# Optimization experiments

Hardware: AMD Instinct MI355X
Metric: run time of the kernel (lower is better)

The kernel has to match this reference:

```python
import jax, jax.numpy as jnp
import numpy as np

NUM_LEVELS = 16
FEATS_PER_LEVEL = 2
LOG2_HASHMAP = 19
TABLE_SIZE = 1 << LOG2_HASHMAP
BASE_RES = 16
DESIRED_RES = 4096
PER_LEVEL_SCALE = float(np.exp(np.log(DESIRED_RES / BASE_RES) / (NUM_LEVELS - 1)))
PRIMES = (np.uint32(1), np.uint32(2654435761), np.uint32(805459861))
N_POINTS = 2_000_000


def _level_features(x, table, level):
    # x: [N,3] in [0,1]; table: [TABLE_SIZE, F]
    scale = BASE_RES * (PER_LEVEL_SCALE ** level) - 1.0
    res = int(np.ceil(scale)) + 1
    dense = (res ** 3) <= TABLE_SIZE  # tcnn uses dense indexing when grid fits
    pos = x * scale + 0.5
    pos0 = jnp.floor(pos)
    w = pos - pos0                     # trilinear weights, [N,3]
    base = pos0.astype(jnp.uint32)
    out = jnp.zeros((x.shape[0], table.shape[1]), dtype=table.dtype)
    for c in range(8):                 # 8 corners of the voxel
        offs = [(c >> d) & 1 for d in range(3)]
        pc = [jnp.minimum(base[:, d] + np.uint32(offs[d]), np.uint32(res - 1)) for d in range(3)]
        if dense:
            idx = pc[0] + pc[1] * np.uint32(res) + pc[2] * np.uint32(res * res)
        else:
            idx = (pc[0] * PRIMES[0]) ^ (pc[1] * PRIMES[1]) ^ (pc[2] * PRIMES[2])
            idx = idx & np.uint32(TABLE_SIZE - 1)
        wt = jnp.ones(x.shape[0], dtype=x.dtype)
        for d in range(3):
            wt = wt * (w[:, d] if offs[d] else (1.0 - w[:, d]))
        out = out + wt[:, None] * table[idx.astype(jnp.int32)]
    return out


def hashgrid_encode(x, tables):
    # x: [N,3] in [0,1]; tables: [L, TABLE_SIZE, F] -> [N, L*F]
    return jnp.concatenate(
        [_level_features(x, tables[l], l) for l in range(NUM_LEVELS)], axis=-1)


def setup_inputs() -> dict:
    key = jax.random.key(0)
    k1, k2, k3, k4, k5 = jax.random.split(key, 5)
    points = jax.random.uniform(k1, (N_POINTS, 3), dtype=jnp.float32)
    # tcnn hashgrid init: uniform(-1e-4, 1e-4)
    tables = jax.random.uniform(k2, (NUM_LEVELS, TABLE_SIZE, FEATS_PER_LEVEL),
                                minval=-1e-4, maxval=1e-4, dtype=jnp.float32)
    def kaiming(k, fan_out, fan_in):
        bound = np.sqrt(2.0) * np.sqrt(3.0 / fan_in)
        return jax.random.uniform(k, (fan_out, fan_in), minval=-bound, maxval=bound,
                                  dtype=jnp.float32)
    W1 = kaiming(k3, 32, 32)
    W2 = kaiming(k4, 32, 32)
    W3 = kaiming(k5, 4, 32)
    aabb = jnp.stack([jnp.zeros(3, jnp.float32), jnp.ones(3, jnp.float32)])
    return {"points": points, "tables": tables, "W1": W1, "W2": W2, "W3": W3,
            "aabb": aabb}


def reference(points, tables, W1, W2, W3, aabb):
    texc = jnp.clip((points - aabb[0][None, :]) / (aabb[1] - aabb[0])[None, :], 0.0, 1.0)
    enc = hashgrid_encode(texc, tables)            # [N, 32]
    h = jax.nn.relu(enc @ W1.T)
    h = jax.nn.relu(h @ W2.T)
    out = h @ W3.T                                 # [N, 4]
    mn = jnp.array([0.0, 0.0, 0.0, 0.01], dtype=out.dtype)
    mx = jnp.array([1.0, 1.0, 1.0, 1.0], dtype=out.dtype)
    return jax.nn.sigmoid(out) * (mx - mn) + mn
```

## Files before the change

kernel.cpp:

```cpp
#include <hip/hip_runtime.h>
#include <cmath>


namespace {
constexpr int kLevels = 16;
constexpr unsigned kTableSize = 1u << 19;
constexpr unsigned kMask = kTableSize - 1u;
constexpr int kNumCells = 1 << 18;
constexpr int kScanBlocks = kNumCells / 256;

typedef _Float16 half2_t __attribute__((ext_vector_type(2)));
typedef unsigned int u32;

struct LevelParams {
  float scale[kLevels];
  unsigned res[kLevels];
  int dense[kLevels];
};
}

__device__ __forceinline__ u32 part1by2(u32 x) {
  x &= 0x3FFu;
  x = (x | (x << 16)) & 0x030000FFu;
  x = (x | (x << 8))  & 0x0300F00Fu;
  x = (x | (x << 4))  & 0x030C30C3u;
  x = (x | (x << 2))  & 0x09249249u;
  return x;
}

__device__ __forceinline__ u32 cell_of(float x, float y, float z) {
  u32 cx = min((u32)(x * 64.f), 63u);
  u32 cy = min((u32)(y * 64.f), 63u);
  u32 cz = min((u32)(z * 64.f), 63u);
  return part1by2(cx) | (part1by2(cy) << 1) | (part1by2(cz) << 2);
}

__global__ __launch_bounds__(256)
void conv_tables_kernel(const float2* __restrict__ src, half2_t* __restrict__ dst,
                        int n_entries,
                        const float* __restrict__ W1, const float* __restrict__ W2,
                        const float* __restrict__ W3, half2_t* __restrict__ Wh)
{
  int i = blockIdx.x * blockDim.x + threadIdx.x;
  if (i < 512) {
    Wh[i] = half2_t{(_Float16)W1[2 * i], (_Float16)W1[2 * i + 1]};
  } else if (i < 1024) {
    int t = i - 512;
    Wh[512 + t] = half2_t{(_Float16)W2[2 * t], (_Float16)W2[2 * t + 1]};
  } else if (i < 1088) {
    int t = i - 1024;
    Wh[1024 + t] = half2_t{(_Float16)W3[2 * t], (_Float16)W3[2 * t + 1]};
  }
  int stride = gridDim.x * blockDim.x;
  for (; i < n_entries; i += stride) {
    float2 v = src[i];
    dst[i] = half2_t{(_Float16)v.x, (_Float16)v.y};
  }
}

__global__ __launch_bounds__(256)
void hist_kernel(const float* __restrict__ points, const float* __restrict__ aabb,
                 u32* __restrict__ hist, int n)
{
  int i = blockIdx.x * blockDim.x + threadIdx.x;
  if (i >= n) return;
  float a0x = aabb[0], a0y = aabb[1], a0z = aabb[2];
  float a1x = aabb[3], a1y = aabb[4], a1z = aabb[5];
  float x = fminf(fmaxf((points[3 * i + 0] - a0x) / (a1x - a0x), 0.f), 1.f);
  float y = fminf(fmaxf((points[3 * i + 1] - a0y) / (a1y - a0y), 0.f), 1.f);
  float z = fminf(fmaxf((points[3 * i + 2] - a0z) / (a1z - a0z), 0.f), 1.f);
  atomicAdd(&hist[cell_of(x, y, z)], 1u);
}

__global__ __launch_bounds__(256)
void scan1_kernel(u32* __restrict__ hist, u32* __restrict__ totals)
{
  __shared__ u32 s[256];
  int t = threadIdx.x;
  int base = blockIdx.x * 256;
  u32 v = hist[base + t];
  s[t] = v;
  __syncthreads();
  #pragma unroll
  for (int off = 1; off < 256; off <<= 1) {
    u32 a = (t >= off) ? s[t - off] : 0u;
    __syncthreads();
    s[t] += a;
    __syncthreads();
  }
  if (t == 255) totals[blockIdx.x] = s[255];
  hist[base + t] = s[t] - v;
}

__global__ __launch_bounds__(1024)
void scan2_kernel(u32* __restrict__ totals)
{
  __shared__ u32 s[kScanBlocks];
  int t = threadIdx.x;
  u32 v = totals[t];
  s[t] = v;
  __syncthreads();
  #pragma unroll
  for (int off = 1; off < kScanBlocks; off <<= 1) {
    u32 a = (t >= off) ? s[t - off] : 0u;
    __syncthreads();
    s[t] += a;
    __syncthreads();
  }
  totals[t] = s[t] - v;
}

__global__ __launch_bounds__(256)
void scan3_kernel(u32* __restrict__ hist, const u32* __restrict__ totals)
{
  int t = threadIdx.x;
  int base = blockIdx.x * 256;
  hist[base + t] += totals[blockIdx.x];
}

__global__ __launch_bounds__(256)
void scatter_kernel(const float* __restrict__ points, const float* __restrict__ aabb,
                    u32* __restrict__ offs,
                    float* __restrict__ sx, float* __restrict__ sy,
                    float* __restrict__ sz, u32* __restrict__ perm, int n)
{
  int i = blockIdx.x * blockDim.x + threadIdx.x;
  if (i >= n) return;
  float a0x = aabb[0], a0y = aabb[1], a0z = aabb[2];
  float a1x = aabb[3], a1y = aabb[4], a1z = aabb[5];
  float x = fminf(fmaxf((points[3 * i + 0] - a0x) / (a1x - a0x), 0.f), 1.f);
  float y = fminf(fmaxf((points[3 * i + 1] - a0y) / (a1y - a0y), 0.f), 1.f);
  float z = fminf(fmaxf((points[3 * i + 2] - a0z) / (a1z - a0z), 0.f), 1.f);
  u32 pos = atomicAdd(&offs[cell_of(x, y, z)], 1u);
  sx[pos] = x; sy[pos] = y; sz[pos] = z;
  perm[pos] = (u32)i;
}

__device__ __forceinline__ u32 sel4(uint4 v, u32 j) {
  u32 lo = (j & 1u) ? v.y : v.x;
  u32 hi = (j & 1u) ? v.w : v.z;
  return (j & 2u) ? hi : lo;
}

__global__ __launch_bounds__(256)
void encode_sorted_kernel(const float* __restrict__ sx, const float* __restrict__ sy,
                          const float* __restrict__ sz,
                          const u32* __restrict__ tables,
                          half2_t* __restrict__ enc,
                          LevelParams lp, int n, int bpl)
{
  int l = blockIdx.x / bpl;
  int i = (blockIdx.x - l * bpl) * blockDim.x + threadIdx.x;
  if (i >= n) return;

  float x = sx[i], y = sy[i], z = sz[i];

  float s = lp.scale[l];
  unsigned res = lp.res[l];
  bool dense = (lp.dense[l] != 0);
  unsigned rm1 = res - 1u;
  unsigned res2 = res * res;
  const u32* tab = tables + (size_t)l * kTableSize;

  float fx = x * s + 0.5f, fy = y * s + 0.5f, fz = z * s + 0.5f;
  float fx0 = floorf(fx), fy0 = floorf(fy), fz0 = floorf(fz);
  float wx = fx - fx0, wy = fy - fy0, wz = fz - fz0;
  unsigned bx = (unsigned)fx0, by = (unsigned)fy0, bz = (unsigned)fz0;

  unsigned pcx0 = min(bx, rm1), pcx1 = min(bx + 1u, rm1);

  u32 idx0[4], idx1[4];
  #pragma unroll
  for (int p = 0; p < 4; ++p) {
    unsigned oy = (unsigned)(p & 1);
    unsigned oz = (unsigned)(p >> 1);
    unsigned pcy = min(by + oy, rm1);
    unsigned pcz = min(bz + oz, rm1);
    if (dense) {
      u32 b = pcy * res + pcz * res2;
      idx0[p] = pcx0 + b;
      idx1[p] = pcx1 + b;
    } else {
      u32 h = (pcy * 2654435761u) ^ (pcz * 805459861u);
      idx0[p] = (pcx0 ^ h) & kMask;
      idx1[p] = (pcx1 ^ h) & kMask;
    }
  }

  uint4 v[4];
  #pragma unroll
  for (int p = 0; p < 4; ++p)
    v[p] = *reinterpret_cast<const uint4*>(tab + (idx0[p] & ~3u));

  u32 e1x[4] = {0u, 0u, 0u, 0u};
  #pragma unroll
  for (int p = 0; p < 4; ++p) {
    if ((idx0[p] ^ idx1[p]) >= 4u) e1x[p] = tab[idx1[p]];
  }

  float wx1 = wx, wx0 = 1.f - wx;
  float acc0 = 0.f, acc1 = 0.f;
  #pragma unroll
  for (int p = 0; p < 4; ++p) {
    unsigned oy = (unsigned)(p & 1);
    unsigned oz = (unsigned)(p >> 1);
    float wyz = (oy ? wy : 1.f - wy) * (oz ? wz : 1.f - wz);
    u32 e0 = sel4(v[p], idx0[p] & 3u);
    u32 e1g = sel4(v[p], idx1[p] & 3u);
    u32 e1 = ((idx0[p] ^ idx1[p]) < 4u) ? e1g : e1x[p];
    half2_t f0 = __builtin_bit_cast(half2_t, e0);
    half2_t f1 = __builtin_bit_cast(half2_t, e1);
    float w0 = wyz * wx0, w1 = wyz * wx1;
    acc0 += w0 * (float)f0.x + w1 * (float)f1.x;
    acc1 += w0 * (float)f0.y + w1 * (float)f1.y;
  }
  enc[(size_t)l * n + i] = half2_t{(_Float16)acc0, (_Float16)acc1};
}

__device__ __forceinline__ float dot2_acc(half2_t a, half2_t b, float c) {
#if __has_builtin(__builtin_amdgcn_fdot2)
  return __builtin_amdgcn_fdot2(a, b, c, false);
#else
  return c + (float)a.x * (float)b.x + (float)a.y * (float)b.y;
#endif
}

__global__ __launch_bounds__(256)
void mlp_kernel(const half2_t* __restrict__ enc,
                const half2_t* __restrict__ Wh,
                const u32* __restrict__ perm,
                float* __restrict__ out, int n)
{
  int i = blockIdx.x * blockDim.x + threadIdx.x;
  if (i >= n) return;

  half2_t e[16];
  #pragma unroll
  for (int l = 0; l < kLevels; ++l) e[l] = enc[(size_t)l * n + i];

  const half2_t* W1h = Wh;
  const half2_t* W2h = Wh + 512;
  const half2_t* W3h = Wh + 1024;

  float h1f[32];
  #pragma unroll
  for (int j = 0; j < 32; ++j) {
    float acc = 0.f;
    #pragma unroll
    for (int k = 0; k < 16; ++k) acc = dot2_acc(e[k], W1h[16 * j + k], acc);
    h1f[j] = fmaxf(acc, 0.f);
  }
  half2_t h1[16];
  #pragma unroll
  for (int k = 0; k < 16; ++k)
    h1[k] = half2_t{(_Float16)h1f[2 * k], (_Float16)h1f[2 * k + 1]};

  float h2f[32];
  #pragma unroll
  for (int j = 0; j < 32; ++j) {
    float acc = 0.f;
    #pragma unroll
    for (int k = 0; k < 16; ++k) acc = dot2_acc(h1[k], W2h[16 * j + k], acc);
    h2f[j] = fmaxf(acc, 0.f);
  }
  half2_t h2[16];
  #pragma unroll
  for (int k = 0; k < 16; ++k)
    h2[k] = half2_t{(_Float16)h2f[2 * k], (_Float16)h2f[2 * k + 1]};

  float o[4];
  #pragma unroll
  for (int j = 0; j < 4; ++j) {
    float acc = 0.f;
    #pragma unroll
    for (int k = 0; k < 16; ++k) acc = dot2_acc(h2[k], W3h[16 * j + k], acc);
    o[j] = acc;
  }

  float4 r;
  r.x = 1.f / (1.f + __expf(-o[0]));
  r.y = 1.f / (1.f + __expf(-o[1]));
  r.z = 1.f / (1.f + __expf(-o[2]));
  r.w = 0.99f / (1.f + __expf(-o[3])) + 0.01f;
  int oi = perm ? (int)perm[i] : i;
  reinterpret_cast<float4*>(out)[oi] = r;
}

__global__ __launch_bounds__(256)
void encode_raw_kernel(const float* __restrict__ points,
                       const u32* __restrict__ tables,
                       const float* __restrict__ aabb,
                       half2_t* __restrict__ enc,
                       LevelParams lp, int n, int bpl)
{
  int l = blockIdx.x / bpl;
  int i = (blockIdx.x - l * bpl) * blockDim.x + threadIdx.x;
  if (i >= n) return;

  float a0x = aabb[0], a0y = aabb[1], a0z = aabb[2];
  float a1x = aabb[3], a1y = aabb[4], a1z = aabb[5];
  float x = fminf(fmaxf((points[3 * i + 0] - a0x) / (a1x - a0x), 0.f), 1.f);
  float y = fminf(fmaxf((points[3 * i + 1] - a0y) / (a1y - a0y), 0.f), 1.f);
  float z = fminf(fmaxf((points[3 * i + 2] - a0z) / (a1z - a0z), 0.f), 1.f);

  float s = lp.scale[l];
  unsigned res = lp.res[l];
  bool dense = (lp.dense[l] != 0);
  unsigned rm1 = res - 1u;
  unsigned res2 = res * res;
  const u32* tab = tables + (size_t)l * kTableSize;

  float fx = x * s + 0.5f, fy = y * s + 0.5f, fz = z * s + 0.5f;
  float fx0 = floorf(fx), fy0 = floorf(fy), fz0 = floorf(fz);
  float wx = fx - fx0, wy = fy - fy0, wz = fz - fz0;
  unsigned bx = (unsigned)fx0, by = (unsigned)fy0, bz = (unsigned)fz0;
  unsigned pcx0 = min(bx, rm1), pcx1 = min(bx + 1u, rm1);

  u32 idx0[4], idx1[4];
  #pragma unroll
  for (int p = 0; p < 4; ++p) {
    unsigned oy = (unsigned)(p & 1);
    unsigned oz = (unsigned)(p >> 1);
    unsigned pcy = min(by + oy, rm1);
    unsigned pcz = min(bz + oz, rm1);
    if (dense) {
      u32 b = pcy * res + pcz * res2;
      idx0[p] = pcx0 + b;
      idx1[p] = pcx1 + b;
    } else {
      u32 h = (pcy * 2654435761u) ^ (pcz * 805459861u);
      idx0[p] = (pcx0 ^ h) & kMask;
      idx1[p] = (pcx1 ^ h) & kMask;
    }
  }
  uint4 v[4];
  #pragma unroll
  for (int p = 0; p < 4; ++p)
    v[p] = *reinterpret_cast<const uint4*>(tab + (idx0[p] & ~3u));
  u32 e1x[4] = {0u, 0u, 0u, 0u};
  #pragma unroll
  for (int p = 0; p < 4; ++p) {
    if ((idx0[p] ^ idx1[p]) >= 4u) e1x[p] = tab[idx1[p]];
  }
  float wx1 = wx, wx0 = 1.f - wx;
  float acc0 = 0.f, acc1 = 0.f;
  #pragma unroll
  for (int p = 0; p < 4; ++p) {
    unsigned oy = (unsigned)(p & 1);
    unsigned oz = (unsigned)(p >> 1);
    float wyz = (oy ? wy : 1.f - wy) * (oz ? wz : 1.f - wz);
    u32 e0 = sel4(v[p], idx0[p] & 3u);
    u32 e1g = sel4(v[p], idx1[p] & 3u);
    u32 e1 = ((idx0[p] ^ idx1[p]) < 4u) ? e1g : e1x[p];
    half2_t f0 = __builtin_bit_cast(half2_t, e0);
    half2_t f1 = __builtin_bit_cast(half2_t, e1);
    float w0 = wyz * wx0, w1 = wyz * wx1;
    acc0 += w0 * (float)f0.x + w1 * (float)f1.x;
    acc1 += w0 * (float)f0.y + w1 * (float)f1.y;
  }
  enc[(size_t)l * n + i] = half2_t{(_Float16)acc0, (_Float16)acc1};
}

__global__ __launch_bounds__(256)
void hashgrid_mlp_kernel(const float* __restrict__ points,
                         const float* __restrict__ tables,
                         const float* __restrict__ W1,
                         const float* __restrict__ W2,
                         const float* __restrict__ W3,
                         const float* __restrict__ aabb,
                         float* __restrict__ out,
                         LevelParams lp, int n)
{
  int i = blockIdx.x * blockDim.x + threadIdx.x;
  if (i >= n) return;
  float a0x = aabb[0], a0y = aabb[1], a0z = aabb[2];
  float a1x = aabb[3], a1y = aabb[4], a1z = aabb[5];
  float x = fminf(fmaxf((points[3 * i + 0] - a0x) / (a1x - a0x), 0.f), 1.f);
  float y = fminf(fmaxf((points[3 * i + 1] - a0y) / (a1y - a0y), 0.f), 1.f);
  float z = fminf(fmaxf((points[3 * i + 2] - a0z) / (a1z - a0z), 0.f), 1.f);
  float enc[2 * kLevels];
  #pragma unroll
  for (int l = 0; l < kLevels; ++l) {
    float s = lp.scale[l];
    unsigned res = lp.res[l];
    bool dense = (lp.dense[l] != 0);
    unsigned rm1 = res - 1u;
    unsigned res2 = res * res;
    float fx = x * s + 0.5f, fy = y * s + 0.5f, fz = z * s + 0.5f;
    float fx0 = floorf(fx), fy0 = floorf(fy), fz0 = floorf(fz);
    float wx = fx - fx0, wy = fy - fy0, wz = fz - fz0;
    unsigned bx = (unsigned)fx0, by = (unsigned)fy0, bz = (unsigned)fz0;
    const float2* tab = reinterpret_cast<const float2*>(tables) + (size_t)l * kTableSize;
    float acc0 = 0.f, acc1 = 0.f;
    #pragma unroll
    for (int c = 0; c < 8; ++c) {
      unsigned ox = (unsigned)(c & 1);
      unsigned oy = (unsigned)((c >> 1) & 1);
      unsigned oz = (unsigned)((c >> 2) & 1);
      unsigned pcx = min(bx + ox, rm1);
      unsigned pcy = min(by + oy, rm1);
      unsigned pcz = min(bz + oz, rm1);
      unsigned idx;
      if (dense) idx = pcx + pcy * res + pcz * res2;
      else idx = (pcx ^ (pcy * 2654435761u) ^ (pcz * 805459861u)) & kMask;
      float wt = (ox ? wx : 1.f - wx) * (oy ? wy : 1.f - wy) * (oz ? wz : 1.f - wz);
      float2 f = tab[idx];
      acc0 += wt * f.x;
      acc1 += wt * f.y;
    }
    enc[2 * l + 0] = acc0;
    enc[2 * l + 1] = acc1;
  }
  float h1[32];
  #pragma unroll
  for (int j = 0; j < 32; ++j) {
    float acc = 0.f;
    #pragma unroll
    for (int k = 0; k < 32; ++k) acc += enc[k] * W1[32 * j + k];
    h1[j] = fmaxf(acc, 0.f);
  }
  float h2[32];
  #pragma unroll
  for (int j = 0; j < 32; ++j) {
    float acc = 0.f;
    #pragma unroll
    for (int k = 0; k < 32; ++k) acc += h1[k] * W2[32 * j + k];
    h2[j] = fmaxf(acc, 0.f);
  }
  float o[4];
  #pragma unroll
  for (int j = 0; j < 4; ++j) {
    float acc = 0.f;
    #pragma unroll
    for (int k = 0; k < 32; ++k) acc += h2[k] * W3[32 * j + k];
    o[j] = acc;
  }
  float4 r;
  r.x = 1.f / (1.f + __expf(-o[0]));
  r.y = 1.f / (1.f + __expf(-o[1]));
  r.z = 1.f / (1.f + __expf(-o[2]));
  r.w = 0.99f / (1.f + __expf(-o[3])) + 0.01f;
  reinterpret_cast<float4*>(out)[i] = r;
}

extern "C" void kernel_launch(void* const* d_in, const int* in_sizes, int n_in,
                              void* d_out, int out_size, void* d_ws, size_t ws_size,
                              hipStream_t stream) {
  const float* points = (const float*)d_in[0];
  const float* tables = (const float*)d_in[1];
  const float* W1     = (const float*)d_in[2];
  const float* W2     = (const float*)d_in[3];
  const float* W3     = (const float*)d_in[4];
  const float* aabb   = (const float*)d_in[5];
  float* out = (float*)d_out;
  int n = in_sizes[0] / 3;

  LevelParams lp;
  const double pls = std::exp(std::log(4096.0 / 16.0) / 15.0);
  for (int l = 0; l < kLevels; ++l) {
    double s = 16.0 * std::pow(pls, (double)l) - 1.0;
    lp.scale[l] = (float)s;
    long long res = (long long)std::ceil(s) + 1;
    lp.res[l] = (unsigned)res;
    lp.dense[l] = (res * res * res <= (long long)kTableSize) ? 1 : 0;
  }

  const int block = 256;
  const int n_entries = kLevels * (int)kTableSize;
  const int grid_n = (n + block - 1) / block;

  auto align256 = [](size_t v) { return (v + 255) & ~(size_t)255; };
  const size_t tab_b   = align256((size_t)n_entries * 4);
  const size_t enc_b   = align256((size_t)kLevels * n * 4);
  const size_t wh_b    = align256(1088 * 4);
  const size_t hist_b  = align256((size_t)kNumCells * 4);
  const size_t tot_b   = align256((size_t)kScanBlocks * 4);
  const size_t sxyz_b  = align256((size_t)n * 4);
  const size_t perm_b  = align256((size_t)n * 4);
  const size_t need_sorted = tab_b + enc_b + wh_b + hist_b + tot_b + 3 * sxyz_b + perm_b;
  const size_t need_r3     = tab_b + enc_b + wh_b;

  if (ws_size >= need_sorted) {
    char* p = (char*)d_ws;
    half2_t* tab_f16 = (half2_t*)p;            p += tab_b;
    half2_t* enc     = (half2_t*)p;            p += enc_b;
    half2_t* Wh      = (half2_t*)p;            p += wh_b;
    u32* hist        = (u32*)p;                p += hist_b;
    u32* totals      = (u32*)p;                p += tot_b;
    float* sx        = (float*)p;              p += sxyz_b;
    float* sy        = (float*)p;              p += sxyz_b;
    float* sz        = (float*)p;              p += sxyz_b;
    u32* perm        = (u32*)p;

    hipMemsetAsync(hist, 0, (size_t)kNumCells * 4, stream);

    conv_tables_kernel<<<2048, block, 0, stream>>>(
        reinterpret_cast<const float2*>(tables), tab_f16, n_entries, W1, W2, W3, Wh);

    hist_kernel<<<grid_n, block, 0, stream>>>(points, aabb, hist, n);
    scan1_kernel<<<kScanBlocks, 256, 0, stream>>>(hist, totals);
    scan2_kernel<<<1, kScanBlocks, 0, stream>>>(totals);
    scan3_kernel<<<kScanBlocks, 256, 0, stream>>>(hist, totals);
    scatter_kernel<<<grid_n, block, 0, stream>>>(points, aabb, hist, sx, sy, sz, perm, n);

    encode_sorted_kernel<<<grid_n * kLevels, block, 0, stream>>>(
        sx, sy, sz, reinterpret_cast<const u32*>(tab_f16), enc, lp, n, grid_n);

    mlp_kernel<<<grid_n, block, 0, stream>>>(enc, Wh, perm, out, n);
  } else if (ws_size >= need_r3) {
    char* p = (char*)d_ws;
    half2_t* tab_f16 = (half2_t*)p;            p += tab_b;
    half2_t* enc     = (half2_t*)p;            p += enc_b;
    half2_t* Wh      = (half2_t*)p;

    conv_tables_kernel<<<2048, block, 0, stream>>>(
        reinterpret_cast<const float2*>(tables), tab_f16, n_entries, W1, W2, W3, Wh);
    encode_raw_kernel<<<grid_n * kLevels, block, 0, stream>>>(
        points, reinterpret_cast<const u32*>(tab_f16), aabb, enc, lp, n, grid_n);
    mlp_kernel<<<grid_n, block, 0, stream>>>(enc, Wh, nullptr, out, n);
  } else {
    hashgrid_mlp_kernel<<<grid_n, block, 0, stream>>>(
        points, tables, W1, W2, W3, aabb, out, lp, n);
  }
}
```

Baseline: 902.7 us.

## Pack sorted coords and permutation into float4 and coarsen sort grid

Replaces the separate x/y/z/perm sorted arrays with a single float4 array, storing the original index in the w lane, so scatter writes one vector and encode/mlp read one vector. It also reduces the Morton sort grid from 64^3 to 32^3 cells, shrinking the histogram and scan work. In exchange, each encode pass reads 16 bytes per point instead of 12, atomics contend more per cell, and sort locality is coarser for the fine levels.

Measured after the change: 961.1 us. +6.5%, slower.

```diff
diff --git a/kernel.cpp b/kernel.cpp
--- a/kernel.cpp
+++ b/kernel.cpp
@@ -6,7 +6,8 @@
 constexpr int kLevels = 16;
 constexpr unsigned kTableSize = 1u << 19;
 constexpr unsigned kMask = kTableSize - 1u;
-constexpr int kNumCells = 1 << 18;
+constexpr int kCellsPow = 15;
+constexpr int kNumCells = 1 << kCellsPow;
 constexpr int kScanBlocks = kNumCells / 256;
 
 typedef _Float16 half2_t __attribute__((ext_vector_type(2)));
@@ -29,9 +30,9 @@
 }
 
 __device__ __forceinline__ u32 cell_of(float x, float y, float z) {
-  u32 cx = min((u32)(x * 64.f), 63u);
-  u32 cy = min((u32)(y * 64.f), 63u);
-  u32 cz = min((u32)(z * 64.f), 63u);
+  u32 cx = min((u32)(x * 32.f), 31u);
+  u32 cy = min((u32)(y * 32.f), 31u);
+  u32 cz = min((u32)(z * 32.f), 31u);
   return part1by2(cx) | (part1by2(cy) << 1) | (part1by2(cz) << 2);
 }
 
@@ -92,7 +93,7 @@
   hist[base + t] = s[t] - v;
 }
 
-__global__ __launch_bounds__(1024)
+__global__ __launch_bounds__(kScanBlocks)
 void scan2_kernel(u32* __restrict__ totals)
 {
   __shared__ u32 s[kScanBlocks];
@@ -120,9 +121,7 @@
 
 __global__ __launch_bounds__(256)
 void scatter_kernel(const float* __restrict__ points, const float* __restrict__ aabb,
-                    u32* __restrict__ offs,
-                    float* __restrict__ sx, float* __restrict__ sy,
-                    float* __restrict__ sz, u32* __restrict__ perm, int n)
+                    u32* __restrict__ offs, float4* __restrict__ sp, int n)
 {
   int i = blockIdx.x * blockDim.x + threadIdx.x;
   if (i >= n) return;
@@ -132,8 +131,7 @@
   float y = fminf(fmaxf((points[3 * i + 1] - a0y) / (a1y - a0y), 0.f), 1.f);
   float z = fminf(fmaxf((points[3 * i + 2] - a0z) / (a1z - a0z), 0.f), 1.f);
   u32 pos = atomicAdd(&offs[cell_of(x, y, z)], 1u);
-  sx[pos] = x; sy[pos] = y; sz[pos] = z;
-  perm[pos] = (u32)i;
+  sp[pos] = make_float4(x, y, z, __uint_as_float((u32)i));
 }
 
 __device__ __forceinline__ u32 sel4(uint4 v, u32 j) {
@@ -143,8 +141,7 @@
 }
 
 __global__ __launch_bounds__(256)
-void encode_sorted_kernel(const float* __restrict__ sx, const float* __restrict__ sy,
-                          const float* __restrict__ sz,
+void encode_sorted_kernel(const float4* __restrict__ sp,
                           const u32* __restrict__ tables,
                           half2_t* __restrict__ enc,
                           LevelParams lp, int n, int bpl)
@@ -153,7 +150,8 @@
   int i = (blockIdx.x - l * bpl) * blockDim.x + threadIdx.x;
   if (i >= n) return;
 
-  float x = sx[i], y = sy[i], z = sz[i];
+  float4 c = sp[i];
+  float x = c.x, y = c.y, z = c.z;
 
   float s = lp.scale[l];
   unsigned res = lp.res[l];
@@ -228,7 +226,7 @@
 __global__ __launch_bounds__(256)
 void mlp_kernel(const half2_t* __restrict__ enc,
                 const half2_t* __restrict__ Wh,
-                const u32* __restrict__ perm,
+                const float4* __restrict__ sp,
                 float* __restrict__ out, int n)
 {
   int i = blockIdx.x * blockDim.x + threadIdx.x;
@@ -282,7 +280,7 @@
   r.y = 1.f / (1.f + __expf(-o[1]));
   r.z = 1.f / (1.f + __expf(-o[2]));
   r.w = 0.99f / (1.f + __expf(-o[3])) + 0.01f;
-  int oi = perm ? (int)perm[i] : i;
+  int oi = sp ? (int)__float_as_uint(sp[i].w) : i;
   reinterpret_cast<float4*>(out)[oi] = r;
 }
 
@@ -475,9 +473,8 @@
   const size_t wh_b    = align256(1088 * 4);
   const size_t hist_b  = align256((size_t)kNumCells * 4);
   const size_t tot_b   = align256((size_t)kScanBlocks * 4);
-  const size_t sxyz_b  = align256((size_t)n * 4);
-  const size_t perm_b  = align256((size_t)n * 4);
-  const size_t need_sorted = tab_b + enc_b + wh_b + hist_b + tot_b + 3 * sxyz_b + perm_b;
+  const size_t sp_b    = align256((size_t)n * 16);
+  const size_t need_sorted = tab_b + enc_b + wh_b + hist_b + tot_b + sp_b;
   const size_t need_r3     = tab_b + enc_b + wh_b;
 
   if (ws_size >= need_sorted) {
@@ -487,10 +484,7 @@
     half2_t* Wh      = (half2_t*)p;            p += wh_b;
     u32* hist        = (u32*)p;                p += hist_b;
     u32* totals      = (u32*)p;                p += tot_b;
-    float* sx        = (float*)p;              p += sxyz_b;
-    float* sy        = (float*)p;              p += sxyz_b;
-    float* sz        = (float*)p;              p += sxyz_b;
-    u32* perm        = (u32*)p;
+    float4* sp       = (float4*)p;
 
     hipMemsetAsync(hist, 0, (size_t)kNumCells * 4, stream);
 
@@ -501,12 +495,12 @@
     scan1_kernel<<<kScanBlocks, 256, 0, stream>>>(hist, totals);
     scan2_kernel<<<1, kScanBlocks, 0, stream>>>(totals);
     scan3_kernel<<<kScanBlocks, 256, 0, stream>>>(hist, totals);
-    scatter_kernel<<<grid_n, block, 0, stream>>>(points, aabb, hist, sx, sy, sz, perm, n);
+    scatter_kernel<<<grid_n, block, 0, stream>>>(points, aabb, hist, sp, n);
 
     encode_sorted_kernel<<<grid_n * kLevels, block, 0, stream>>>(
-        sx, sy, sz, reinterpret_cast<const u32*>(tab_f16), enc, lp, n, grid_n);
-
-    mlp_kernel<<<grid_n, block, 0, stream>>>(enc, Wh, perm, out, n);
+        sp, reinterpret_cast<const u32*>(tab_f16), enc, lp, n, grid_n);
+
+    mlp_kernel<<<grid_n, block, 0, stream>>>(enc, Wh, sp, out, n);
   } else if (ws_size >= need_r3) {
     char* p = (char*)d_ws;
     half2_t* tab_f16 = (half2_t*)p;            p += tab_b;
```
